# Kernel optimization log

Hardware: AMD Instinct MI355X
Metric: run time of the kernel (lower is better)

## Reference

```python
import jax, jax.numpy as jnp
import numpy as np

N_NODES = 50000
N_EDGES = 800000
NODE_F = 100     # memory_feats
EDGE_F = 100     # raw edge feature dim
TIME_D = 100     # temporal encoder dimension
HEADS = 2
OUT_F = 100
NEG_SLOPE = 0.2


def setup_inputs() -> dict:
    key = jax.random.key(0)
    ks = jax.random.split(key, 16)
    return {
        'memory': jax.random.normal(ks[0], (N_NODES, NODE_F), jnp.float32),
        'node_ts': jax.random.uniform(ks[1], (N_NODES,), jnp.float32),
        'edge_feats_raw': jax.random.normal(ks[2], (N_EDGES, EDGE_F), jnp.float32),
        'edge_ts': jax.random.uniform(ks[3], (N_EDGES,), jnp.float32),
        'time_w': jax.random.normal(ks[4], (TIME_D,), jnp.float32),
        'time_b': jax.random.normal(ks[5], (TIME_D,), jnp.float32),
        'fc_node_w': jax.random.normal(ks[6], (NODE_F, HEADS * OUT_F), jnp.float32) * 0.1,
        'fc_node_b': jax.random.normal(ks[7], (HEADS * OUT_F,), jnp.float32) * 0.1,
        'fc_edge_w': jax.random.normal(ks[8], (EDGE_F + TIME_D, HEADS * OUT_F), jnp.float32) * 0.1,
        'fc_edge_b': jax.random.normal(ks[9], (HEADS * OUT_F,), jnp.float32) * 0.1,
        'attn_l': jax.random.normal(ks[10], (HEADS, OUT_F), jnp.float32) * 0.1,
        'attn_r': jax.random.normal(ks[11], (HEADS, OUT_F), jnp.float32) * 0.1,
        'attn_e': jax.random.normal(ks[12], (HEADS, OUT_F), jnp.float32) * 0.1,
        'src': jax.random.randint(ks[13], (N_EDGES,), 0, N_NODES, jnp.int32),
        'dst': jax.random.randint(ks[14], (N_EDGES,), 0, N_NODES, jnp.int32),
    }


def _forward(memory, node_ts, edge_feats_raw, edge_ts,
             time_w, time_b, fc_node_w, fc_node_b, fc_edge_w, fc_edge_b,
             attn_l, attn_r, attn_e, src, dst):
    n = memory.shape[0]
    # TemporalEdgePreprocess: Fourier time encoding of (edge_ts - ts[src])
    time_diff = edge_ts - node_ts[src]                                  # [E]
    te = jnp.cos(time_diff[:, None] * time_w[None, :] + time_b[None, :])  # [E, T]
    efeat = jnp.concatenate([edge_feats_raw, te], axis=1)               # [E, EDGE_F+T]

    # EdgeGATConv (eval mode: dropouts are identity)
    node_feat = (memory @ fc_node_w + fc_node_b).reshape(n, HEADS, OUT_F)          # [N,H,F]
    edge_feat = (efeat @ fc_edge_w + fc_edge_b).reshape(-1, HEADS, OUT_F)          # [E,H,F]

    el = jnp.einsum('nhf,hf->nh', node_feat, attn_l)   # [N,H]
    er = jnp.einsum('nhf,hf->nh', node_feat, attn_r)   # [N,H]
    ee = jnp.einsum('ehf,hf->eh', edge_feat, attn_e)   # [E,H]

    el_prime = el[src] + ee                             # u_add_e  [E,H]
    e = el_prime + er[dst]                              # e_add_v  [E,H]
    e = jnp.where(e > 0, e, NEG_SLOPE * e)              # leaky_relu

    # edge_softmax: softmax over incoming edges per destination node, per head
    emax = jax.ops.segment_max(e, dst, num_segments=n)  # [N,H]
    emax = jnp.where(jnp.isfinite(emax), emax, 0.0)     # zero-in-degree safety
    e_exp = jnp.exp(e - emax[dst])                      # [E,H]
    denom = jax.ops.segment_sum(e_exp, dst, num_segments=n)  # [N,H]
    a = e_exp / denom[dst]                              # [E,H]

    # msg_fn: m = a * el_prime (el_prime has singleton feature dim in torch code)
    m = a * el_prime                                    # [E,H]
    ft = jax.ops.segment_sum(m, dst, num_segments=n)    # [N,H]  (== [N,H,1] features)

    # residual: Identity since memory_feats == out_feats -> view(N,-1,F) = [N,1,F]
    rst = ft[:, :, None] + memory[:, None, :]           # [N,H,F] via broadcast
    return rst.mean(axis=1)                             # .mean(1) over heads -> [N,F]


def reference(memory, node_ts, edge_feats_raw, edge_ts,
              time_w, time_b, fc_node_w, fc_node_b, fc_edge_w, fc_edge_b,
              attn_l, attn_r, attn_e, src, dst):
    return _forward(memory, node_ts, edge_feats_raw, edge_ts,
                    time_w, time_b, fc_node_w, fc_node_b, fc_edge_w, fc_edge_b,
                    attn_l, attn_r, attn_e, src, dst)
```

## Files before the change

### kernel.cpp

```cpp
#include <hip/hip_runtime.h>


constexpr int F = 100;
constexpr float NEG_SLOPE = 0.2f;
constexpr int EPB = 32;

__device__ __forceinline__ float wave_reduce(float v) {
#pragma unroll
    for (int off = 32; off > 0; off >>= 1)
        v += __shfl_down(v, off, 64);
    return v;
}

__global__ void precompute_kernel(
    const float* __restrict__ fc_node_w, const float* __restrict__ fc_node_b,
    const float* __restrict__ fc_edge_w, const float* __restrict__ fc_edge_b,
    const float* __restrict__ attn_l, const float* __restrict__ attn_r,
    const float* __restrict__ attn_e,
    float4* __restrict__ w_node, float2* __restrict__ w_edge,
    float* __restrict__ bias,
    int* __restrict__ cnt, int N)
{
    int wid  = blockIdx.x * (blockDim.x >> 6) + (threadIdx.x >> 6);
    int lane = threadIdx.x & 63;
    if (wid < F) {
        int t = wid;
        float a0 = 0.f, a1 = 0.f, a2 = 0.f, a3 = 0.f;
        for (int f = lane; f < F; f += 64) {
            float w0 = fc_node_w[t * 2 * F + f];
            float w1 = fc_node_w[t * 2 * F + F + f];
            a0 += w0 * attn_l[f];
            a1 += w1 * attn_l[F + f];
            a2 += w0 * attn_r[f];
            a3 += w1 * attn_r[F + f];
        }
        a0 = wave_reduce(a0); a1 = wave_reduce(a1);
        a2 = wave_reduce(a2); a3 = wave_reduce(a3);
        if (lane == 0) w_node[t] = make_float4(a0, a1, a2, a3);
    } else if (wid < 3 * F) {
        int t = wid - F;
        float a0 = 0.f, a1 = 0.f;
        for (int f = lane; f < F; f += 64) {
            a0 += fc_edge_w[t * 2 * F + f] * attn_e[f];
            a1 += fc_edge_w[t * 2 * F + F + f] * attn_e[F + f];
        }
        a0 = wave_reduce(a0); a1 = wave_reduce(a1);
        if (lane == 0) w_edge[t] = make_float2(a0, a1);
    } else if (wid < 3 * F + 6) {
        int j = wid - 3 * F;
        const float* b  = (j < 4) ? fc_node_b : fc_edge_b;
        const float* av = (j < 2) ? attn_l : (j < 4 ? attn_r : attn_e);
        int h = j & 1;
        float a0 = 0.f;
        for (int f = lane; f < F; f += 64)
            a0 += b[h * F + f] * av[h * F + f];
        a0 = wave_reduce(a0);
        if (lane == 0) bias[j] = a0;
    }
    for (int i = blockIdx.x * blockDim.x + threadIdx.x; i < N;
         i += gridDim.x * blockDim.x)
        cnt[i] = 0;
}

__global__ void node_count_kernel(const float* __restrict__ memory,
                                  const float4* __restrict__ w_node,
                                  const float* __restrict__ bias,
                                  float4* __restrict__ el_er,
                                  const int* __restrict__ dst,
                                  int* __restrict__ cnt,
                                  int N, int E, int nodeBlocks)
{
    if ((int)blockIdx.x < nodeBlocks) {
        int n    = blockIdx.x * (blockDim.x >> 6) + (threadIdx.x >> 6);
        int lane = threadIdx.x & 63;
        if (n >= N) return;
        const float* mrow = memory + (size_t)n * F;
        float a0 = 0.f, a1 = 0.f, a2 = 0.f, a3 = 0.f;
        for (int k = lane; k < F; k += 64) {
            float m  = mrow[k];
            float4 w = w_node[k];
            a0 += m * w.x; a1 += m * w.y; a2 += m * w.z; a3 += m * w.w;
        }
        a0 = wave_reduce(a0); a1 = wave_reduce(a1);
        a2 = wave_reduce(a2); a3 = wave_reduce(a3);
        if (lane == 0)
            el_er[n] = make_float4(a0 + bias[0], a1 + bias[1],
                                   a2 + bias[2], a3 + bias[3]);
    } else {
        int i = (blockIdx.x - nodeBlocks) * blockDim.x + threadIdx.x;
        if (i < E) atomicAdd(&cnt[dst[i]], 1);
    }
}

__global__ void scan1_kernel(const int* __restrict__ cnt,
                             int* __restrict__ offs,
                             int* __restrict__ bsum, int N)
{
    __shared__ int tmp[256];
    int i = blockIdx.x * 256 + threadIdx.x;
    int v = (i < N) ? cnt[i] : 0;
    tmp[threadIdx.x] = v;
    __syncthreads();
    for (int d = 1; d < 256; d <<= 1) {
        int t = (threadIdx.x >= d) ? tmp[threadIdx.x - d] : 0;
        __syncthreads();
        tmp[threadIdx.x] += t;
        __syncthreads();
    }
    if (i < N) offs[i] = tmp[threadIdx.x] - v;
    if (threadIdx.x == 255) bsum[blockIdx.x] = tmp[255];
}

__global__ void scan23_kernel(int* __restrict__ offs,
                              const int* __restrict__ bsum,
                              int* __restrict__ cursor, int N, int nb)
{
    __shared__ int tmp[256];
    int t = threadIdx.x;
    int v = (t < nb) ? bsum[t] : 0;
    tmp[t] = v;
    __syncthreads();
    for (int d = 1; d < 256; d <<= 1) {
        int x = (t >= d) ? tmp[t - d] : 0;
        __syncthreads();
        tmp[t] += x;
        __syncthreads();
    }
    int boff = (blockIdx.x == 0) ? 0 : tmp[blockIdx.x - 1];
    int i = blockIdx.x * 256 + t;
    if (i < N) {
        int o = offs[i] + boff;
        offs[i]   = o;
        cursor[i] = o;
    }
}

__global__ void edge_gemv_kernel(
    const float* __restrict__ edge_raw,
    const float* __restrict__ edge_ts,
    const float* __restrict__ node_ts,
    const int* __restrict__ src,
    const int* __restrict__ dst,
    const float* __restrict__ time_w,
    const float* __restrict__ time_b,
    const float2* __restrict__ w_edge,
    const float* __restrict__ bias,
    const float4* __restrict__ el_er,
    int* __restrict__ cursor,
    float4* __restrict__ bucket, int E)
{
    __shared__ float4 wx4[25], wy4[25], wz4[25], ww4[25], tw4[25], tb4[25];
    __shared__ float  td_s[EPB];
    __shared__ float2 el_s[EPB];
    __shared__ float2 er_s[EPB];
    __shared__ int    d_s[EPB];

    const int  t  = threadIdx.x;
    const long eb = (long)blockIdx.x * EPB;

    if (t < 25) {
        float4 x, y, z, w, tw, tb;
#pragma unroll
        for (int j = 0; j < 4; ++j) {
            int k = 4 * t + j;
            float2 wr = w_edge[k];
            float2 wt = w_edge[F + k];
            ((float*)&x)[j]  = wr.x;  ((float*)&y)[j]  = wr.y;
            ((float*)&z)[j]  = wt.x;  ((float*)&w)[j]  = wt.y;
            ((float*)&tw)[j] = time_w[k];
            ((float*)&tb)[j] = time_b[k];
        }
        wx4[t] = x; wy4[t] = y; wz4[t] = z; ww4[t] = w;
        tw4[t] = tw; tb4[t] = tb;
    } else if (t >= 64 && t < 64 + EPB) {
        int  l = t - 64;
        long e = eb + l;
        if (e < E) {
            int s = src[e], d = dst[e];
            d_s[l]  = d;
            td_s[l] = edge_ts[e] - node_ts[s];
            float4 a = el_er[s];
            float4 b = el_er[d];
            el_s[l] = make_float2(a.x, a.y);
            er_s[l] = make_float2(b.z, b.w);
        }
    }
    __syncthreads();

    const int  el_ = t >> 3;
    const int  s8  = t & 7;
    const long e   = eb + el_;
    float a0 = 0.f, a1 = 0.f;
    if (e < E) {
        const float  td   = td_s[el_];
        const float4* row = (const float4*)edge_raw + e * 25;
#pragma unroll
        for (int i = 0; i < 4; ++i) {
            int c = s8 + 8 * i;
            if (c < 25) {
                float4 r  = row[c];
                float4 x  = wx4[c], y = wy4[c], z = wz4[c], w = ww4[c];
                float4 tw = tw4[c], tb = tb4[c];
                float c0 = __cosf(fmaf(td, tw.x, tb.x));
                float c1 = __cosf(fmaf(td, tw.y, tb.y));
                float c2 = __cosf(fmaf(td, tw.z, tb.z));
                float c3 = __cosf(fmaf(td, tw.w, tb.w));
                a0 = fmaf(r.x, x.x, fmaf(c0, z.x, a0));
                a1 = fmaf(r.x, y.x, fmaf(c0, w.x, a1));
                a0 = fmaf(r.y, x.y, fmaf(c1, z.y, a0));
                a1 = fmaf(r.y, y.y, fmaf(c1, w.y, a1));
                a0 = fmaf(r.z, x.z, fmaf(c2, z.z, a0));
                a1 = fmaf(r.z, y.z, fmaf(c2, w.z, a1));
                a0 = fmaf(r.w, x.w, fmaf(c3, z.w, a0));
                a1 = fmaf(r.w, y.w, fmaf(c3, w.w, a1));
            }
        }
    }
    a0 += __shfl_down(a0, 4, 64);  a1 += __shfl_down(a1, 4, 64);
    a0 += __shfl_down(a0, 2, 64);  a1 += __shfl_down(a1, 2, 64);
    a0 += __shfl_down(a0, 1, 64);  a1 += __shfl_down(a1, 1, 64);

    if (s8 == 0 && e < E) {
        float elp0 = el_s[el_].x + a0 + bias[4];
        float elp1 = el_s[el_].y + a1 + bias[5];
        float e0 = elp0 + er_s[el_].x;
        float e1 = elp1 + er_s[el_].y;
        e0 = e0 > 0.f ? e0 : NEG_SLOPE * e0;
        e1 = e1 > 0.f ? e1 : NEG_SLOPE * e1;
        float x0 = __expf(e0);
        float x1 = __expf(e1);
        int pos = atomicAdd(&cursor[d_s[el_]], 1);
        bucket[pos] = make_float4(x0 * elp0, x1 * elp1, x0, x1);
    }
}

__global__ void reduce_out_kernel(const float4* __restrict__ bucket,
                                  const int* __restrict__ offs,
                                  const int* __restrict__ cnt,
                                  const float* __restrict__ memory,
                                  float* __restrict__ out, int N)
{
    int g = blockIdx.x * (blockDim.x >> 4) + (threadIdx.x >> 4);
    int l = threadIdx.x & 15;
    if (g >= N) return;
    int base = offs[g];
    int deg  = cnt[g];
    float s0 = 0.f, s1 = 0.f, s2 = 0.f, s3 = 0.f;
    for (int j = l; j < deg; j += 16) {
        float4 v = bucket[base + j];
        s0 += v.x; s1 += v.y; s2 += v.z; s3 += v.w;
    }
    s0 += __shfl_down(s0, 8, 64); s1 += __shfl_down(s1, 8, 64);
    s2 += __shfl_down(s2, 8, 64); s3 += __shfl_down(s3, 8, 64);
    s0 += __shfl_down(s0, 4, 64); s1 += __shfl_down(s1, 4, 64);
    s2 += __shfl_down(s2, 4, 64); s3 += __shfl_down(s3, 4, 64);
    s0 += __shfl_down(s0, 2, 64); s1 += __shfl_down(s1, 2, 64);
    s2 += __shfl_down(s2, 2, 64); s3 += __shfl_down(s3, 2, 64);
    s0 += __shfl_down(s0, 1, 64); s1 += __shfl_down(s1, 1, 64);
    s2 += __shfl_down(s2, 1, 64); s3 += __shfl_down(s3, 1, 64);
    float ft0 = (s2 != 0.f) ? s0 / s2 : 0.f;
    float ft1 = (s3 != 0.f) ? s1 / s3 : 0.f;
    float add = 0.5f * (ft0 + ft1);
    add = __shfl(add, 0, 16);

    const float4* m4 = (const float4*)(memory + (size_t)g * F);
    float4*       o4 = (float4*)(out + (size_t)g * F);
#pragma unroll
    for (int c = l; c < F / 4; c += 16) {
        float4 m = m4[c];
        float4 o;
        o.x = m.x + add; o.y = m.y + add;
        o.z = m.z + add; o.w = m.w + add;
        o4[c] = o;
    }
}

extern "C" void kernel_launch(void* const* d_in, const int* in_sizes, int n_in,
                              void* d_out, int out_size, void* d_ws, size_t ws_size,
                              hipStream_t stream)
{
    const float* memory     = (const float*)d_in[0];
    const float* node_ts    = (const float*)d_in[1];
    const float* edge_raw   = (const float*)d_in[2];
    const float* edge_ts    = (const float*)d_in[3];
    const float* time_w     = (const float*)d_in[4];
    const float* time_b     = (const float*)d_in[5];
    const float* fc_node_w  = (const float*)d_in[6];
    const float* fc_node_b  = (const float*)d_in[7];
    const float* fc_edge_w  = (const float*)d_in[8];
    const float* fc_edge_b  = (const float*)d_in[9];
    const float* attn_l     = (const float*)d_in[10];
    const float* attn_r     = (const float*)d_in[11];
    const float* attn_e     = (const float*)d_in[12];
    const int*   src        = (const int*)d_in[13];
    const int*   dst        = (const int*)d_in[14];
    float*       out        = (float*)d_out;

    const int N = in_sizes[1];
    const int E = in_sizes[3];

    float* ws = (float*)d_ws;
    float4* w_node  = (float4*)ws;
    float2* w_edge  = (float2*)(ws + 400);
    float*  bias    = ws + 800;
    float4* el_er   = (float4*)(ws + 816);
    int*    cnt     = (int*)(ws + 816 + 5 * (size_t)N);
    int*    offs    = cnt + N;
    int*    cursor  = offs + N;
    int*    bsum    = cursor + N;
    size_t  boff    = 816 + 8 * (size_t)N + 256;
    boff            = (boff + 3) & ~(size_t)3;
    float4* bucket  = (float4*)(ws + boff);

    const int nb = (N + 255) / 256;

    {
        int wblocks = (3 * F + 6 + 3) / 4;
        int blocks  = (nb > wblocks) ? nb : wblocks;
        precompute_kernel<<<blocks, 256, 0, stream>>>(
            fc_node_w, fc_node_b, fc_edge_w, fc_edge_b,
            attn_l, attn_r, attn_e, w_node, w_edge, bias, cnt, N);
    }
    {
        int nodeBlocks  = (N + 3) / 4;
        int countBlocks = (E + 255) / 256;
        node_count_kernel<<<nodeBlocks + countBlocks, 256, 0, stream>>>(
            memory, w_node, bias, el_er, dst, cnt, N, E, nodeBlocks);
    }
    scan1_kernel<<<nb, 256, 0, stream>>>(cnt, offs, bsum, N);
    scan23_kernel<<<nb, 256, 0, stream>>>(offs, bsum, cursor, N, nb);
    {
        int blocks = (E + EPB - 1) / EPB;
        edge_gemv_kernel<<<blocks, 256, 0, stream>>>(
            edge_raw, edge_ts, node_ts, src, dst, time_w, time_b,
            w_edge, bias, el_er, cursor, bucket, E);
    }
    {
        int blocks = (N + 15) / 16;
        reduce_out_kernel<<<blocks, 256, 0, stream>>>(
            bucket, offs, cnt, memory, out, N);
    }
}
```

Before: 547.3 us.

## Replace CSR bucketing and segmented reduce with direct float atomic accumulation

Removes the in-degree count, the two prefix-scan kernels and the per-edge bucket write plus per-node segmented reduction. Each edge instead atomically adds its weighted message and softmax weight into a per-destination float4 accumulator, and a final kernel divides and adds the residual. This cuts launches and memory traffic for the bucket. In exchange it uses four float atomics per edge and makes the summation order nondeterministic.

```diff
diff --git a/kernel.cpp b/kernel.cpp
--- a/kernel.cpp
+++ b/kernel.cpp
@@ -19,7 +19,7 @@
     const float* __restrict__ attn_e,
     float4* __restrict__ w_node, float2* __restrict__ w_edge,
     float* __restrict__ bias,
-    int* __restrict__ cnt, int N)
+    float* __restrict__ accum, int N)
 {
     int wid  = blockIdx.x * (blockDim.x >> 6) + (threadIdx.x >> 6);
     int lane = threadIdx.x & 63;
@@ -57,82 +57,32 @@
         a0 = wave_reduce(a0);
         if (lane == 0) bias[j] = a0;
     }
-    for (int i = blockIdx.x * blockDim.x + threadIdx.x; i < N;
+    int total = 4 * N;
+    for (int i = blockIdx.x * blockDim.x + threadIdx.x; i < total;
          i += gridDim.x * blockDim.x)
-        cnt[i] = 0;
-}
-
-__global__ void node_count_kernel(const float* __restrict__ memory,
-                                  const float4* __restrict__ w_node,
-                                  const float* __restrict__ bias,
-                                  float4* __restrict__ el_er,
-                                  const int* __restrict__ dst,
-                                  int* __restrict__ cnt,
-                                  int N, int E, int nodeBlocks)
-{
-    if ((int)blockIdx.x < nodeBlocks) {
-        int n    = blockIdx.x * (blockDim.x >> 6) + (threadIdx.x >> 6);
-        int lane = threadIdx.x & 63;
-        if (n >= N) return;
-        const float* mrow = memory + (size_t)n * F;
-        float a0 = 0.f, a1 = 0.f, a2 = 0.f, a3 = 0.f;
-        for (int k = lane; k < F; k += 64) {
-            float m  = mrow[k];
-            float4 w = w_node[k];
-            a0 += m * w.x; a1 += m * w.y; a2 += m * w.z; a3 += m * w.w;
-        }
-        a0 = wave_reduce(a0); a1 = wave_reduce(a1);
-        a2 = wave_reduce(a2); a3 = wave_reduce(a3);
-        if (lane == 0)
-            el_er[n] = make_float4(a0 + bias[0], a1 + bias[1],
-                                   a2 + bias[2], a3 + bias[3]);
-    } else {
-        int i = (blockIdx.x - nodeBlocks) * blockDim.x + threadIdx.x;
-        if (i < E) atomicAdd(&cnt[dst[i]], 1);
-    }
-}
-
-__global__ void scan1_kernel(const int* __restrict__ cnt,
-                             int* __restrict__ offs,
-                             int* __restrict__ bsum, int N)
-{
-    __shared__ int tmp[256];
-    int i = blockIdx.x * 256 + threadIdx.x;
-    int v = (i < N) ? cnt[i] : 0;
-    tmp[threadIdx.x] = v;
-    __syncthreads();
-    for (int d = 1; d < 256; d <<= 1) {
-        int t = (threadIdx.x >= d) ? tmp[threadIdx.x - d] : 0;
-        __syncthreads();
-        tmp[threadIdx.x] += t;
-        __syncthreads();
-    }
-    if (i < N) offs[i] = tmp[threadIdx.x] - v;
-    if (threadIdx.x == 255) bsum[blockIdx.x] = tmp[255];
-}
-
-__global__ void scan23_kernel(int* __restrict__ offs,
-                              const int* __restrict__ bsum,
-                              int* __restrict__ cursor, int N, int nb)
-{
-    __shared__ int tmp[256];
-    int t = threadIdx.x;
-    int v = (t < nb) ? bsum[t] : 0;
-    tmp[t] = v;
-    __syncthreads();
-    for (int d = 1; d < 256; d <<= 1) {
-        int x = (t >= d) ? tmp[t - d] : 0;
-        __syncthreads();
-        tmp[t] += x;
-        __syncthreads();
-    }
-    int boff = (blockIdx.x == 0) ? 0 : tmp[blockIdx.x - 1];
-    int i = blockIdx.x * 256 + t;
-    if (i < N) {
-        int o = offs[i] + boff;
-        offs[i]   = o;
-        cursor[i] = o;
-    }
+        accum[i] = 0.f;
+}
+
+__global__ void node_kernel(const float* __restrict__ memory,
+                            const float4* __restrict__ w_node,
+                            const float* __restrict__ bias,
+                            float4* __restrict__ el_er, int N)
+{
+    int n    = blockIdx.x * (blockDim.x >> 6) + (threadIdx.x >> 6);
+    int lane = threadIdx.x & 63;
+    if (n >= N) return;
+    const float* mrow = memory + (size_t)n * F;
+    float a0 = 0.f, a1 = 0.f, a2 = 0.f, a3 = 0.f;
+    for (int k = lane; k < F; k += 64) {
+        float m  = mrow[k];
+        float4 w = w_node[k];
+        a0 += m * w.x; a1 += m * w.y; a2 += m * w.z; a3 += m * w.w;
+    }
+    a0 = wave_reduce(a0); a1 = wave_reduce(a1);
+    a2 = wave_reduce(a2); a3 = wave_reduce(a3);
+    if (lane == 0)
+        el_er[n] = make_float4(a0 + bias[0], a1 + bias[1],
+                               a2 + bias[2], a3 + bias[3]);
 }
 
 __global__ void edge_gemv_kernel(
@@ -146,8 +96,7 @@
     const float2* __restrict__ w_edge,
     const float* __restrict__ bias,
     const float4* __restrict__ el_er,
-    int* __restrict__ cursor,
-    float4* __restrict__ bucket, int E)
+    float* __restrict__ accum, int E)
 {
     __shared__ float4 wx4[25], wy4[25], wz4[25], ww4[25], tw4[25], tb4[25];
     __shared__ float  td_s[EPB];
@@ -229,39 +178,25 @@
         e1 = e1 > 0.f ? e1 : NEG_SLOPE * e1;
         float x0 = __expf(e0);
         float x1 = __expf(e1);
-        int pos = atomicAdd(&cursor[d_s[el_]], 1);
-        bucket[pos] = make_float4(x0 * elp0, x1 * elp1, x0, x1);
-    }
-}
-
-__global__ void reduce_out_kernel(const float4* __restrict__ bucket,
-                                  const int* __restrict__ offs,
-                                  const int* __restrict__ cnt,
-                                  const float* __restrict__ memory,
-                                  float* __restrict__ out, int N)
+        float* acc = accum + 4 * (size_t)d_s[el_];
+        atomicAdd(acc + 0, x0 * elp0);
+        atomicAdd(acc + 1, x1 * elp1);
+        atomicAdd(acc + 2, x0);
+        atomicAdd(acc + 3, x1);
+    }
+}
+
+__global__ void out_kernel(const float4* __restrict__ accum,
+                           const float* __restrict__ memory,
+                           float* __restrict__ out, int N)
 {
     int g = blockIdx.x * (blockDim.x >> 4) + (threadIdx.x >> 4);
     int l = threadIdx.x & 15;
     if (g >= N) return;
-    int base = offs[g];
-    int deg  = cnt[g];
-    float s0 = 0.f, s1 = 0.f, s2 = 0.f, s3 = 0.f;
-    for (int j = l; j < deg; j += 16) {
-        float4 v = bucket[base + j];
-        s0 += v.x; s1 += v.y; s2 += v.z; s3 += v.w;
-    }
-    s0 += __shfl_down(s0, 8, 64); s1 += __shfl_down(s1, 8, 64);
-    s2 += __shfl_down(s2, 8, 64); s3 += __shfl_down(s3, 8, 64);
-    s0 += __shfl_down(s0, 4, 64); s1 += __shfl_down(s1, 4, 64);
-    s2 += __shfl_down(s2, 4, 64); s3 += __shfl_down(s3, 4, 64);
-    s0 += __shfl_down(s0, 2, 64); s1 += __shfl_down(s1, 2, 64);
-    s2 += __shfl_down(s2, 2, 64); s3 += __shfl_down(s3, 2, 64);
-    s0 += __shfl_down(s0, 1, 64); s1 += __shfl_down(s1, 1, 64);
-    s2 += __shfl_down(s2, 1, 64); s3 += __shfl_down(s3, 1, 64);
-    float ft0 = (s2 != 0.f) ? s0 / s2 : 0.f;
-    float ft1 = (s3 != 0.f) ? s1 / s3 : 0.f;
+    float4 a = accum[g];
+    float ft0 = (a.z != 0.f) ? a.x / a.z : 0.f;
+    float ft1 = (a.w != 0.f) ? a.y / a.w : 0.f;
     float add = 0.5f * (ft0 + ft1);
-    add = __shfl(add, 0, 16);
 
     const float4* m4 = (const float4*)(memory + (size_t)g * F);
     float4*       o4 = (float4*)(out + (size_t)g * F);
@@ -304,40 +239,30 @@
     float2* w_edge  = (float2*)(ws + 400);
     float*  bias    = ws + 800;
     float4* el_er   = (float4*)(ws + 816);
-    int*    cnt     = (int*)(ws + 816 + 5 * (size_t)N);
-    int*    offs    = cnt + N;
-    int*    cursor  = offs + N;
-    int*    bsum    = cursor + N;
-    size_t  boff    = 816 + 8 * (size_t)N + 256;
-    boff            = (boff + 3) & ~(size_t)3;
-    float4* bucket  = (float4*)(ws + boff);
-
-    const int nb = (N + 255) / 256;
+    float*  accum   = ws + 816 + 4 * (size_t)N;
 
     {
         int wblocks = (3 * F + 6 + 3) / 4;
-        int blocks  = (nb > wblocks) ? nb : wblocks;
+        int zblocks = (4 * N + 255) / 256;
+        int blocks  = (zblocks > wblocks) ? zblocks : wblocks;
         precompute_kernel<<<blocks, 256, 0, stream>>>(
             fc_node_w, fc_node_b, fc_edge_w, fc_edge_b,
-            attn_l, attn_r, attn_e, w_node, w_edge, bias, cnt, N);
-    }
-    {
-        int nodeBlocks  = (N + 3) / 4;
-        int countBlocks = (E + 255) / 256;
-        node_count_kernel<<<nodeBlocks + countBlocks, 256, 0, stream>>>(
-            memory, w_node, bias, el_er, dst, cnt, N, E, nodeBlocks);
-    }
-    scan1_kernel<<<nb, 256, 0, stream>>>(cnt, offs, bsum, N);
-    scan23_kernel<<<nb, 256, 0, stream>>>(offs, bsum, cursor, N, nb);
+            attn_l, attn_r, attn_e, w_node, w_edge, bias, accum, N);
+    }
+    {
+        int blocks = (N + 3) / 4;
+        node_kernel<<<blocks, 256, 0, stream>>>(
+            memory, w_node, bias, el_er, N);
+    }
     {
         int blocks = (E + EPB - 1) / EPB;
         edge_gemv_kernel<<<blocks, 256, 0, stream>>>(
             edge_raw, edge_ts, node_ts, src, dst, time_w, time_b,
-            w_edge, bias, el_er, cursor, bucket, E);
+            w_edge, bias, el_er, accum, E);
     }
     {
         int blocks = (N + 15) / 16;
-        reduce_out_kernel<<<blocks, 256, 0, stream>>>(
-            bucket, offs, cnt, memory, out, N);
-    }
-}
+        out_kernel<<<blocks, 256, 0, stream>>>(
+            (const float4*)accum, memory, out, N);
+    }
+}
```

After: 555.3 us. About the same (+1.5%).
